# Performance work log

Hardware: AMD Instinct MI355X
Metric: run time of the kernel (lower is better)

## Reference

```python
import jax, jax.numpy as jnp
import numpy as np

B, T, D_IN, D_OUT = 4, 2048, 1024, 1024


def setup_inputs() -> dict:
    key = jax.random.key(0)
    k0, k1, k2, k3 = jax.random.split(key, 4)
    token_embed = jax.random.normal(k0, (B, T, D_IN), dtype=jnp.float32)
    # torch Linear weight is [out, in]; store transposed [in, out] for x @ W
    Wq = jax.random.normal(k1, (D_IN, D_OUT), dtype=jnp.float32) * (1.0 / np.sqrt(D_IN))
    Wk = jax.random.normal(k2, (D_IN, D_OUT), dtype=jnp.float32) * (1.0 / np.sqrt(D_IN))
    Wv = jax.random.normal(k3, (D_IN, D_OUT), dtype=jnp.float32) * (1.0 / np.sqrt(D_IN))
    return {"token_embed": token_embed, "Wq": Wq, "Wk": Wk, "Wv": Wv}


def reference(token_embed, Wq, Wk, Wv):
    # token_embed: [B, T, d_in]
    num_token = token_embed.shape[1]
    q = jnp.einsum("btd,de->bte", token_embed, Wq)  # [B, T, d_out]
    k = jnp.einsum("btd,de->bte", token_embed, Wk)
    v = jnp.einsum("btd,de->bte", token_embed, Wv)
    scores = jnp.einsum("bqe,bke->bqk", q, k)  # [B, T, T]
    # causal mask: strictly-upper-triangular positions set to -inf
    causal = jnp.triu(jnp.ones((num_token, num_token), dtype=bool), k=1)
    scores = jnp.where(causal[None, :, :], -jnp.inf, scores)
    # NOTE: faithful to source bug: scale by sqrt(seq_len) (keys.shape[1]), not sqrt(d_out)
    scale = jnp.asarray(num_token, dtype=scores.dtype) ** 0.5
    attn = jax.nn.softmax(scores / scale, axis=-1)
    # dropout prob is 0 -> identity
    context = jnp.einsum("bqk,bke->bqe", attn, v)  # [B, T, d_out]
    return context
```

## Files before the change

kernel.cpp:

```cpp
#include <hip/hip_runtime.h>
#include <cstdint>
#include <cstddef>
#include <math.h>


typedef __attribute__((ext_vector_type(4))) float f32x4;
typedef __attribute__((ext_vector_type(8))) short s16x8;

#define AS1(p) ((const __attribute__((address_space(1))) void*)(p))
#define AS3(p) ((__attribute__((address_space(3))) void*)(p))
#define BARRIER() asm volatile("s_barrier" ::: "memory")
#define W8 asm volatile("s_waitcnt vmcnt(8)" ::: "memory")
#define W4 asm volatile("s_waitcnt vmcnt(4)" ::: "memory")
#define W0 asm volatile("s_waitcnt vmcnt(0)" ::: "memory")
#define WNONE ((void)0)
#define NOISSUE ((void)0)

static __device__ __forceinline__ unsigned short f2bf(float x) {
  unsigned int u = __float_as_uint(x);
  unsigned int r = u + 0x7FFFu + ((u >> 16) & 1u);
  return (unsigned short)(r >> 16);
}
static __device__ __forceinline__ float bf2f(unsigned short h) {
  return __uint_as_float(((unsigned int)h) << 16);
}

__global__ __launch_bounds__(256) void k_cvtX(const float* __restrict__ X,
                                              unsigned short* __restrict__ Xb) {
  size_t i = ((size_t)blockIdx.x * 256 + threadIdx.x) * 8;
  float4 a = *(const float4*)(X + i);
  float4 b = *(const float4*)(X + i + 4);
  union { unsigned short us[8]; uint4 v; } o;
  o.us[0] = f2bf(a.x); o.us[1] = f2bf(a.y); o.us[2] = f2bf(a.z); o.us[3] = f2bf(a.w);
  o.us[4] = f2bf(b.x); o.us[5] = f2bf(b.y); o.us[6] = f2bf(b.z); o.us[7] = f2bf(b.w);
  *(uint4*)(Xb + i) = o.v;
}

__global__ __launch_bounds__(256) void k_cvtW(const float* __restrict__ W0p,
                                              const float* __restrict__ W1p,
                                              const float* __restrict__ W2p,
                                              unsigned short* __restrict__ Wt) {
  const float* W = blockIdx.z == 0 ? W0p : (blockIdx.z == 1 ? W1p : W2p);
  unsigned short* dst = Wt + (size_t)blockIdx.z * 1024 * 1024;
  __shared__ float tile[64][65];
  int k0 = blockIdx.x * 64, n0 = blockIdx.y * 64;
  int tr = threadIdx.x >> 4, tc = (threadIdx.x & 15) * 4;
  for (int i = 0; i < 4; ++i) {
    int r = tr + i * 16;
    float4 v = *(const float4*)(W + (size_t)(k0 + r) * 1024 + n0 + tc);
    tile[r][tc + 0] = v.x; tile[r][tc + 1] = v.y;
    tile[r][tc + 2] = v.z; tile[r][tc + 3] = v.w;
  }
  __syncthreads();
  for (int i = 0; i < 4; ++i) {
    int r = tr + i * 16;
    ushort4 o;
    o.x = f2bf(tile[tc + 0][r]); o.y = f2bf(tile[tc + 1][r]);
    o.z = f2bf(tile[tc + 2][r]); o.w = f2bf(tile[tc + 3][r]);
    *(ushort4*)(dst + (size_t)(n0 + r) * 1024 + k0 + tc) = o;
  }
}

static __device__ __forceinline__ void stage2(const char* src, size_t ld128, char* dst) {
  __builtin_amdgcn_global_load_lds(AS1(src), AS3(dst), 16, 0, 0);
  __builtin_amdgcn_global_load_lds(AS1(src + ld128), AS3(dst + 8192), 16, 0, 0);
}

template <class FA, class FB>
static __device__ __forceinline__ void core256(const char* __restrict__ As,
                                               const char* __restrict__ Bs,
                                               size_t ldA128, size_t ldB128,
                                               FA offA, FB offB,
                                               int nkt, char* smem, f32x4 (&acc)[8][4]) {
  const int tid = threadIdx.x, w = tid >> 6, lane = tid & 63;
  const int lr = lane & 15, lq = lane >> 4;
  const int wm = (w >> 2) * 128, wn = (w & 3) * 64;
  char* ldsA = smem + w * 1024;
  char* ldsB = smem + 65536 + w * 1024;
  s16x8 af[4], bfr[4];

#define STG_A(t, h) stage2(As + offA((t), (h)), ldA128, ldsA + (((t) & 1) * 2 + (h)) * 16384)
#define STG_B(t, h) stage2(Bs + offB((t), (h)), ldB128, ldsB + (((t) & 1) * 2 + (h)) * 16384)
#define RD_A(buf, h, r) (*(const s16x8*)(smem + ((buf) * 2 + (h)) * 16384 + (r) * 64 + ((lq ^ (((r) >> 1) & 3)) << 4)))
#define RD_B(buf, h, r) (*(const s16x8*)(smem + 65536 + ((buf) * 2 + (h)) * 16384 + (r) * 64 + ((lq ^ (((r) >> 1) & 3)) << 4)))
#define ISS_H1(T) do { STG_A((T) + 1, 1); STG_B((T) + 1, 1); } while (0)
#define ISS_H0(T) do { STG_A((T) + 2, 0); STG_B((T) + 2, 0); } while (0)
#define MFMA_Q(base)                                                                     \
  _Pragma("unroll") for (int i = 0; i < 4; ++i)                                          \
  _Pragma("unroll") for (int c = 0; c < 4; ++c)                                          \
    acc[(base) + i][c] = __builtin_amdgcn_mfma_f32_16x16x32_bf16(af[i], bfr[c], acc[(base) + i][c], 0, 0, 0)
#define PH02(buf, h, ISSUE)                                                              \
  _Pragma("unroll") for (int i = 0; i < 4; ++i) af[i] = RD_A(buf, h, wm + i * 16 + lr);  \
  _Pragma("unroll") for (int c = 0; c < 4; ++c) bfr[c] = RD_B(buf, h, wn + c * 16 + lr); \
  ISSUE; BARRIER();                                                                      \
  __builtin_amdgcn_s_setprio(1); MFMA_Q(0); __builtin_amdgcn_s_setprio(0);               \
  BARRIER();
#define PH13(buf, h, WAIT)                                                               \
  _Pragma("unroll") for (int i = 0; i < 4; ++i) af[i] = RD_A(buf, h, wm + 64 + i * 16 + lr); \
  BARRIER();                                                                             \
  __builtin_amdgcn_s_setprio(1); MFMA_Q(4); __builtin_amdgcn_s_setprio(0);               \
  WAIT; BARRIER();
#define TILE(T, ISS0, ISS2, WAIT1, WAIT3) {                                              \
    const int _buf = (T) & 1;                                                            \
    PH02(_buf, 0, ISS0)                                                                  \
    PH13(_buf, 0, WAIT1)                                                                 \
    PH02(_buf, 1, ISS2)                                                                  \
    PH13(_buf, 1, WAIT3)                                                                 \
  }

  STG_A(0, 0); STG_B(0, 0);
  STG_A(0, 1); STG_B(0, 1);
  STG_A(1, 0); STG_B(1, 0);
  W8; BARRIER();

  int t = 0;
  for (; t + 2 < nkt; ++t) TILE(t, ISS_H1(t), ISS_H0(t), W8, W8)
  TILE(t, ISS_H1(t), NOISSUE, W8, W4)
  ++t;
  TILE(t, NOISSUE, NOISSUE, W0, WNONE)

#undef STG_A
#undef STG_B
#undef RD_A
#undef RD_B
#undef ISS_H1
#undef ISS_H0
#undef MFMA_Q
#undef PH02
#undef PH13
#undef TILE
}

struct OffLinear {
  __device__ __forceinline__ size_t operator()(int t, int h) const {
    return (size_t)t * 128 + (size_t)h * 64;
  }
};
struct OffTri {
  __device__ __forceinline__ size_t operator()(int t, int h) const {
    return (size_t)(t >> 2) * 131072 + (size_t)(t & 3) * 128 + (size_t)h * 64;
  }
};

static __device__ __forceinline__ void lane_src(int ld, int& rowl, int& slot) {
  const int tid = threadIdx.x, w = tid >> 6, lane = tid & 63;
  rowl = w * 16 + (lane >> 2);
  slot = (lane & 3) ^ ((rowl >> 1) & 3);
  (void)ld;
}

__global__ __launch_bounds__(512, 2) void k_qkv(const unsigned short* __restrict__ Xb,
                                                const unsigned short* __restrict__ Wt,
                                                unsigned short* __restrict__ Qm,
                                                unsigned short* __restrict__ Km,
                                                unsigned short* __restrict__ Vt) {
  __shared__ char smem[131072];
  const int by = blockIdx.y, z = by >> 2, q = by & 3, bx = blockIdx.x;
  const char* A; const char* B;
  int m0, n0;
  if (z < 2) {
    m0 = bx * 256; n0 = q * 256;
    A = (const char*)(Xb + (size_t)m0 * 1024);
    B = (const char*)(Wt + (size_t)z * 1048576 + (size_t)n0 * 1024);
  } else {
    m0 = q * 256; n0 = bx * 256;
    A = (const char*)(Wt + (size_t)2 * 1048576 + (size_t)m0 * 1024);
    B = (const char*)(Xb + (size_t)n0 * 1024);
  }
  int rowl, slot; lane_src(2048, rowl, slot);
  const size_t lo = (size_t)rowl * 2048 + slot * 16;
  f32x4 acc[8][4];
#pragma unroll
  for (int i = 0; i < 8; ++i)
#pragma unroll
    for (int c = 0; c < 4; ++c) acc[i][c] = (f32x4){0.f, 0.f, 0.f, 0.f};
  core256(A + lo, B + lo, (size_t)128 * 2048, (size_t)128 * 2048,
          OffLinear{}, OffLinear{}, 16, smem, acc);
  const int tid = threadIdx.x, w = tid >> 6, lane = tid & 63;
  const int lr = lane & 15, lq = lane >> 4;
  const int wm = (w >> 2) * 128, wn = (w & 3) * 64;
#pragma unroll
  for (int fr = 0; fr < 8; ++fr)
#pragma unroll
    for (int fc = 0; fc < 4; ++fc)
#pragma unroll
      for (int i = 0; i < 4; ++i) {
        int row = m0 + wm + fr * 16 + lq * 4 + i;
        int col = n0 + wn + fc * 16 + lr;
        unsigned short hv = f2bf(acc[fr][fc][i]);
        if (z == 0)      Qm[(size_t)row * 1024 + col] = hv;
        else if (z == 1) Km[(size_t)row * 1024 + col] = hv;
        else             Vt[((size_t)(col >> 11) * 1024 + row) * 2048 + (col & 2047)] = hv;
      }
}

__global__ __launch_bounds__(512, 2) void k_sg(const unsigned short* __restrict__ Qm,
                                               const unsigned short* __restrict__ Km,
                                               unsigned short* __restrict__ S) {
  __shared__ char smem[131072];
  const int id = blockIdx.x;
  int i = 0;
  while ((i + 1) * (i + 2) / 2 <= id) ++i;
  const int j = id - i * (i + 1) / 2;
  const int b = blockIdx.y;
  const int m0 = i * 256, n0 = j * 256;
  int rowl, slot; lane_src(2048, rowl, slot);
  const size_t lo = (size_t)rowl * 2048 + slot * 16;
  f32x4 acc[8][4];
#pragma unroll
  for (int a = 0; a < 8; ++a)
#pragma unroll
    for (int c = 0; c < 4; ++c) acc[a][c] = (f32x4){0.f, 0.f, 0.f, 0.f};
  core256((const char*)(Qm + ((size_t)b * 2048 + m0) * 1024) + lo,
          (const char*)(Km + ((size_t)b * 2048 + n0) * 1024) + lo,
          (size_t)128 * 2048, (size_t)128 * 2048, OffLinear{}, OffLinear{}, 16, smem, acc);
  const float SCALE = 0.022097086912079608f;
  const int tid = threadIdx.x, w = tid >> 6, lane = tid & 63;
  const int lr = lane & 15, lq = lane >> 4;
  const int wm = (w >> 2) * 128, wn = (w & 3) * 64;
  unsigned short* tb = S + (((size_t)(b * 36 + id)) << 16);
#pragma unroll
  for (int fr = 0; fr < 8; ++fr)
#pragma unroll
    for (int fc = 0; fc < 4; ++fc)
#pragma unroll
      for (int i2 = 0; i2 < 4; ++i2) {
        int rl = wm + fr * 16 + lq * 4 + i2;
        int cl = wn + fc * 16 + lr;
        tb[(size_t)rl * 256 + cl] = f2bf(acc[fr][fc][i2] * SCALE);
      }
}

__global__ __launch_bounds__(256) void k_softmax(unsigned short* __restrict__ S) {
  const int tid = threadIdx.x, w = tid >> 6, lane = tid & 63;
  const int row = blockIdx.x * 4 + w;
  const int b = row >> 11, q = row & 2047;
  const int i = q >> 8, ntl = i + 1, rowL = q & 255;
  unsigned short* base = S + (((size_t)(b * 36 + (i * (i + 1)) / 2)) << 16)
                           + (size_t)rowL * 256 + lane * 4;
  float v[8][4];
#pragma unroll
  for (int t = 0; t < 8; ++t) {
    if (t < ntl) {
      ushort4 x = *(const ushort4*)(base + (size_t)t * 65536);
      int c0 = t * 256 + lane * 4;
      v[t][0] = (c0 + 0 <= q) ? bf2f(x.x) : -INFINITY;
      v[t][1] = (c0 + 1 <= q) ? bf2f(x.y) : -INFINITY;
      v[t][2] = (c0 + 2 <= q) ? bf2f(x.z) : -INFINITY;
      v[t][3] = (c0 + 3 <= q) ? bf2f(x.w) : -INFINITY;
    } else {
      v[t][0] = v[t][1] = v[t][2] = v[t][3] = -INFINITY;
    }
  }
  float m = -INFINITY;
#pragma unroll
  for (int t = 0; t < 8; ++t)
#pragma unroll
    for (int jj = 0; jj < 4; ++jj) m = fmaxf(m, v[t][jj]);
  for (int off = 32; off; off >>= 1) m = fmaxf(m, __shfl_xor(m, off));
  float s = 0.f;
#pragma unroll
  for (int t = 0; t < 8; ++t)
#pragma unroll
    for (int jj = 0; jj < 4; ++jj) { v[t][jj] = __expf(v[t][jj] - m); s += v[t][jj]; }
  for (int off = 32; off; off >>= 1) s += __shfl_xor(s, off);
  const float inv = 1.f / s;
#pragma unroll
  for (int t = 0; t < 8; ++t)
    if (t < ntl) {
      ushort4 o;
      o.x = f2bf(v[t][0] * inv); o.y = f2bf(v[t][1] * inv);
      o.z = f2bf(v[t][2] * inv); o.w = f2bf(v[t][3] * inv);
      *(ushort4*)(base + (size_t)t * 65536) = o;
    }
}

__global__ __launch_bounds__(512, 2) void k_pv(const unsigned short* __restrict__ P,
                                               const unsigned short* __restrict__ Vt,
                                               float* __restrict__ out) {
  __shared__ char smem[131072];
  const int mtr = 7 - blockIdx.x;
  const int nt = blockIdx.y, b = blockIdx.z;
  const int nkt = (mtr + 1) * 4;
  const char* Pb = (const char*)P + (((size_t)(b * 36 + (mtr * (mtr + 1)) / 2)) << 17);
  int rowl, slot; lane_src(0, rowl, slot);
  const char* Asrc = Pb + (size_t)rowl * 512 + slot * 16;
  const char* Bsrc = (const char*)Vt + ((size_t)(b * 1024 + nt * 256 + rowl)) * 4096 + slot * 16;
  f32x4 acc[8][4];
#pragma unroll
  for (int a = 0; a < 8; ++a)
#pragma unroll
    for (int c = 0; c < 4; ++c) acc[a][c] = (f32x4){0.f, 0.f, 0.f, 0.f};
  core256(Asrc, Bsrc, (size_t)128 * 512, (size_t)128 * 4096,
          OffTri{}, OffLinear{}, nkt, smem, acc);
  const int tid = threadIdx.x, w = tid >> 6, lane = tid & 63;
  const int lr = lane & 15, lq = lane >> 4;
  const int wm = (w >> 2) * 128, wn = (w & 3) * 64;
#pragma unroll
  for (int fr = 0; fr < 8; ++fr)
#pragma unroll
    for (int fc = 0; fc < 4; ++fc)
#pragma unroll
      for (int i2 = 0; i2 < 4; ++i2) {
        int orow = mtr * 256 + wm + fr * 16 + lq * 4 + i2;
        int col = nt * 256 + wn + fc * 16 + lr;
        out[((size_t)b * 2048 + orow) * 1024 + col] = acc[fr][fc][i2];
      }
}

extern "C" void kernel_launch(void* const* d_in, const int* in_sizes, int n_in,
                              void* d_out, int out_size, void* d_ws, size_t ws_size,
                              hipStream_t stream) {
  const float* X  = (const float*)d_in[0];
  const float* W0p = (const float*)d_in[1];
  const float* W1p = (const float*)d_in[2];
  const float* W2p = (const float*)d_in[3];
  float* out = (float*)d_out;
  char* ws = (char*)d_ws;
  unsigned short* Xb = (unsigned short*)ws;
  unsigned short* Wt = (unsigned short*)(ws + (size_t)16777216);
  unsigned short* Qm = (unsigned short*)(ws + (size_t)23068672);
  unsigned short* Km = (unsigned short*)(ws + (size_t)39845888);
  unsigned short* Vt = (unsigned short*)(ws + (size_t)56623104);
  unsigned short* Sb = (unsigned short*)ws;
  (void)in_sizes; (void)n_in; (void)out_size; (void)ws_size;

  hipLaunchKernelGGL(k_cvtX, dim3(4096), dim3(256), 0, stream, X, Xb);
  hipLaunchKernelGGL(k_cvtW, dim3(16, 16, 3), dim3(256), 0, stream, W0p, W1p, W2p, Wt);
  hipLaunchKernelGGL(k_qkv, dim3(32, 12), dim3(512), 0, stream, Xb, Wt, Qm, Km, Vt);
  hipLaunchKernelGGL(k_sg, dim3(36, 4), dim3(512), 0, stream, Qm, Km, Sb);
  hipLaunchKernelGGL(k_softmax, dim3(2048), dim3(256), 0, stream, Sb);
  hipLaunchKernelGGL(k_pv, dim3(8, 4, 4), dim3(512), 0, stream, Sb, Vt, out);
}
```

Baseline: 179.9 us.

## Move V projection into score kernel and split PV over K with atomics

The V projection GEMM moves out of the QKV kernel and into the score-GEMM launch, so the two run concurrently as one grid of 272 blocks (Q/K projection is now 256 blocks). The PV kernel is split along the key dimension into 32 roughly equal chunks per (batch, column tile), using lookup tables, and partial results are accumulated into the output with float atomics after a memset. This balances the triangular causal workload across more CUs and removes the long tail from the largest row tiles. In exchange it adds an output memset, atomic-add traffic, and nondeterministic summation order.

```diff
diff --git a/kernel.cpp b/kernel.cpp
--- a/kernel.cpp
+++ b/kernel.cpp
@@ -136,38 +136,36 @@
     return (size_t)t * 128 + (size_t)h * 64;
   }
 };
-struct OffTri {
+struct OffTriK {
+  int k0;
   __device__ __forceinline__ size_t operator()(int t, int h) const {
-    return (size_t)(t >> 2) * 131072 + (size_t)(t & 3) * 128 + (size_t)h * 64;
+    int g = k0 + t;
+    return (size_t)(g >> 2) * 131072 + (size_t)(g & 3) * 128 + (size_t)h * 64;
   }
 };
-
-static __device__ __forceinline__ void lane_src(int ld, int& rowl, int& slot) {
+struct OffLinK {
+  int k0;
+  __device__ __forceinline__ size_t operator()(int t, int h) const {
+    return (size_t)(k0 + t) * 128 + (size_t)h * 64;
+  }
+};
+
+static __device__ __forceinline__ void lane_src(int& rowl, int& slot) {
   const int tid = threadIdx.x, w = tid >> 6, lane = tid & 63;
   rowl = w * 16 + (lane >> 2);
   slot = (lane & 3) ^ ((rowl >> 1) & 3);
-  (void)ld;
-}
-
-__global__ __launch_bounds__(512, 2) void k_qkv(const unsigned short* __restrict__ Xb,
-                                                const unsigned short* __restrict__ Wt,
-                                                unsigned short* __restrict__ Qm,
-                                                unsigned short* __restrict__ Km,
-                                                unsigned short* __restrict__ Vt) {
+}
+
+__global__ __launch_bounds__(512, 2) void k_qk(const unsigned short* __restrict__ Xb,
+                                               const unsigned short* __restrict__ Wt,
+                                               unsigned short* __restrict__ Qm,
+                                               unsigned short* __restrict__ Km) {
   __shared__ char smem[131072];
   const int by = blockIdx.y, z = by >> 2, q = by & 3, bx = blockIdx.x;
-  const char* A; const char* B;
-  int m0, n0;
-  if (z < 2) {
-    m0 = bx * 256; n0 = q * 256;
-    A = (const char*)(Xb + (size_t)m0 * 1024);
-    B = (const char*)(Wt + (size_t)z * 1048576 + (size_t)n0 * 1024);
-  } else {
-    m0 = q * 256; n0 = bx * 256;
-    A = (const char*)(Wt + (size_t)2 * 1048576 + (size_t)m0 * 1024);
-    B = (const char*)(Xb + (size_t)n0 * 1024);
-  }
-  int rowl, slot; lane_src(2048, rowl, slot);
+  const int m0 = bx * 256, n0 = q * 256;
+  const char* A = (const char*)(Xb + (size_t)m0 * 1024);
+  const char* B = (const char*)(Wt + (size_t)z * 1048576 + (size_t)n0 * 1024);
+  int rowl, slot; lane_src(rowl, slot);
   const size_t lo = (size_t)rowl * 2048 + slot * 16;
   f32x4 acc[8][4];
 #pragma unroll
@@ -176,6 +174,7 @@
     for (int c = 0; c < 4; ++c) acc[i][c] = (f32x4){0.f, 0.f, 0.f, 0.f};
   core256(A + lo, B + lo, (size_t)128 * 2048, (size_t)128 * 2048,
           OffLinear{}, OffLinear{}, 16, smem, acc);
+  unsigned short* C = z == 0 ? Qm : Km;
   const int tid = threadIdx.x, w = tid >> 6, lane = tid & 63;
   const int lr = lane & 15, lq = lane >> 4;
   const int wm = (w >> 2) * 128, wn = (w & 3) * 64;
@@ -187,48 +186,68 @@
       for (int i = 0; i < 4; ++i) {
         int row = m0 + wm + fr * 16 + lq * 4 + i;
         int col = n0 + wn + fc * 16 + lr;
-        unsigned short hv = f2bf(acc[fr][fc][i]);
-        if (z == 0)      Qm[(size_t)row * 1024 + col] = hv;
-        else if (z == 1) Km[(size_t)row * 1024 + col] = hv;
-        else             Vt[((size_t)(col >> 11) * 1024 + row) * 2048 + (col & 2047)] = hv;
+        C[(size_t)row * 1024 + col] = f2bf(acc[fr][fc][i]);
       }
 }
 
-__global__ __launch_bounds__(512, 2) void k_sg(const unsigned short* __restrict__ Qm,
-                                               const unsigned short* __restrict__ Km,
-                                               unsigned short* __restrict__ S) {
+__global__ __launch_bounds__(512, 2) void k_sgv(const unsigned short* __restrict__ Xb,
+                                                const unsigned short* __restrict__ Wt,
+                                                const unsigned short* __restrict__ Qm,
+                                                const unsigned short* __restrict__ Km,
+                                                unsigned short* __restrict__ Vt,
+                                                unsigned short* __restrict__ S) {
   __shared__ char smem[131072];
-  const int id = blockIdx.x;
-  int i = 0;
-  while ((i + 1) * (i + 2) / 2 <= id) ++i;
-  const int j = id - i * (i + 1) / 2;
-  const int b = blockIdx.y;
-  const int m0 = i * 256, n0 = j * 256;
-  int rowl, slot; lane_src(2048, rowl, slot);
+  const int x = blockIdx.x;
+  int rowl, slot; lane_src(rowl, slot);
   const size_t lo = (size_t)rowl * 2048 + slot * 16;
   f32x4 acc[8][4];
 #pragma unroll
   for (int a = 0; a < 8; ++a)
 #pragma unroll
     for (int c = 0; c < 4; ++c) acc[a][c] = (f32x4){0.f, 0.f, 0.f, 0.f};
-  core256((const char*)(Qm + ((size_t)b * 2048 + m0) * 1024) + lo,
-          (const char*)(Km + ((size_t)b * 2048 + n0) * 1024) + lo,
-          (size_t)128 * 2048, (size_t)128 * 2048, OffLinear{}, OffLinear{}, 16, smem, acc);
-  const float SCALE = 0.022097086912079608f;
   const int tid = threadIdx.x, w = tid >> 6, lane = tid & 63;
   const int lr = lane & 15, lq = lane >> 4;
   const int wm = (w >> 2) * 128, wn = (w & 3) * 64;
-  unsigned short* tb = S + (((size_t)(b * 36 + id)) << 16);
-#pragma unroll
-  for (int fr = 0; fr < 8; ++fr)
-#pragma unroll
-    for (int fc = 0; fc < 4; ++fc)
-#pragma unroll
-      for (int i2 = 0; i2 < 4; ++i2) {
-        int rl = wm + fr * 16 + lq * 4 + i2;
-        int cl = wn + fc * 16 + lr;
-        tb[(size_t)rl * 256 + cl] = f2bf(acc[fr][fc][i2] * SCALE);
-      }
+
+  if (x < 128) {
+    const int m0 = (x & 3) * 256, n0 = (x >> 2) * 256;
+    const char* A = (const char*)(Wt + (size_t)2 * 1048576 + (size_t)m0 * 1024);
+    const char* B = (const char*)(Xb + (size_t)n0 * 1024);
+    core256(A + lo, B + lo, (size_t)128 * 2048, (size_t)128 * 2048,
+            OffLinear{}, OffLinear{}, 16, smem, acc);
+#pragma unroll
+    for (int fr = 0; fr < 8; ++fr)
+#pragma unroll
+      for (int fc = 0; fc < 4; ++fc)
+#pragma unroll
+        for (int i = 0; i < 4; ++i) {
+          int row = m0 + wm + fr * 16 + lq * 4 + i;
+          int col = n0 + wn + fc * 16 + lr;
+          Vt[((size_t)(col >> 11) * 1024 + row) * 2048 + (col & 2047)] = f2bf(acc[fr][fc][i]);
+        }
+  } else {
+    const int id2 = x - 128;
+    const int b = id2 / 36, id = id2 % 36;
+    int i = 0;
+    while ((i + 1) * (i + 2) / 2 <= id) ++i;
+    const int j = id - i * (i + 1) / 2;
+    const int m0 = i * 256, n0 = j * 256;
+    core256((const char*)(Qm + ((size_t)b * 2048 + m0) * 1024) + lo,
+            (const char*)(Km + ((size_t)b * 2048 + n0) * 1024) + lo,
+            (size_t)128 * 2048, (size_t)128 * 2048, OffLinear{}, OffLinear{}, 16, smem, acc);
+    const float SCALE = 0.022097086912079608f;
+    unsigned short* tb = S + (((size_t)(b * 36 + id)) << 16);
+#pragma unroll
+    for (int fr = 0; fr < 8; ++fr)
+#pragma unroll
+      for (int fc = 0; fc < 4; ++fc)
+#pragma unroll
+        for (int i2 = 0; i2 < 4; ++i2) {
+          int rl = wm + fr * 16 + lq * 4 + i2;
+          int cl = wn + fc * 16 + lr;
+          tb[(size_t)rl * 256 + cl] = f2bf(acc[fr][fc][i2] * SCALE);
+        }
+  }
 }
 
 __global__ __launch_bounds__(256) void k_softmax(unsigned short* __restrict__ S) {
@@ -275,15 +294,19 @@
     }
 }
 
+__device__ const int pv_i[32]  = {7,7,7,7,7,7,7, 6,6,6,6,6,6, 5,5,5,5,5, 4,4,4,4, 3,3,3,3, 2,2,2, 1,1, 0};
+__device__ const int pv_k0[32] = {0,5,10,15,20,24,28, 0,5,10,15,20,24, 0,5,10,15,20, 0,5,10,15, 0,4,8,12, 0,4,8, 0,4, 0};
+__device__ const int pv_nk[32] = {5,5,5,5,4,4,4, 5,5,5,5,4,4, 5,5,5,5,4, 5,5,5,5, 4,4,4,4, 4,4,4, 4,4, 4};
+
 __global__ __launch_bounds__(512, 2) void k_pv(const unsigned short* __restrict__ P,
                                                const unsigned short* __restrict__ Vt,
                                                float* __restrict__ out) {
   __shared__ char smem[131072];
-  const int mtr = 7 - blockIdx.x;
-  const int nt = blockIdx.y, b = blockIdx.z;
-  const int nkt = (mtr + 1) * 4;
-  const char* Pb = (const char*)P + (((size_t)(b * 36 + (mtr * (mtr + 1)) / 2)) << 17);
-  int rowl, slot; lane_src(0, rowl, slot);
+  const int cx = blockIdx.x & 31;
+  const int nt = (blockIdx.x >> 5) & 3, b = blockIdx.x >> 7;
+  const int i = pv_i[cx], k0 = pv_k0[cx], nkt = pv_nk[cx];
+  const char* Pb = (const char*)P + (((size_t)(b * 36 + (i * (i + 1)) / 2)) << 17);
+  int rowl, slot; lane_src(rowl, slot);
   const char* Asrc = Pb + (size_t)rowl * 512 + slot * 16;
   const char* Bsrc = (const char*)Vt + ((size_t)(b * 1024 + nt * 256 + rowl)) * 4096 + slot * 16;
   f32x4 acc[8][4];
@@ -292,7 +315,7 @@
 #pragma unroll
     for (int c = 0; c < 4; ++c) acc[a][c] = (f32x4){0.f, 0.f, 0.f, 0.f};
   core256(Asrc, Bsrc, (size_t)128 * 512, (size_t)128 * 4096,
-          OffTri{}, OffLinear{}, nkt, smem, acc);
+          OffTriK{k0}, OffLinK{k0}, nkt, smem, acc);
   const int tid = threadIdx.x, w = tid >> 6, lane = tid & 63;
   const int lr = lane & 15, lq = lane >> 4;
   const int wm = (w >> 2) * 128, wn = (w & 3) * 64;
@@ -302,9 +325,9 @@
     for (int fc = 0; fc < 4; ++fc)
 #pragma unroll
       for (int i2 = 0; i2 < 4; ++i2) {
-        int orow = mtr * 256 + wm + fr * 16 + lq * 4 + i2;
+        int orow = i * 256 + wm + fr * 16 + lq * 4 + i2;
         int col = nt * 256 + wn + fc * 16 + lr;
-        out[((size_t)b * 2048 + orow) * 1024 + col] = acc[fr][fc][i2];
+        unsafeAtomicAdd(out + ((size_t)b * 2048 + orow) * 1024 + col, acc[fr][fc][i2]);
       }
 }
 
@@ -323,12 +346,13 @@
   unsigned short* Km = (unsigned short*)(ws + (size_t)39845888);
   unsigned short* Vt = (unsigned short*)(ws + (size_t)56623104);
   unsigned short* Sb = (unsigned short*)ws;
-  (void)in_sizes; (void)n_in; (void)out_size; (void)ws_size;
-
+  (void)in_sizes; (void)n_in; (void)ws_size;
+
+  hipMemsetAsync(out, 0, (size_t)out_size * sizeof(float), stream);
   hipLaunchKernelGGL(k_cvtX, dim3(4096), dim3(256), 0, stream, X, Xb);
   hipLaunchKernelGGL(k_cvtW, dim3(16, 16, 3), dim3(256), 0, stream, W0p, W1p, W2p, Wt);
-  hipLaunchKernelGGL(k_qkv, dim3(32, 12), dim3(512), 0, stream, Xb, Wt, Qm, Km, Vt);
-  hipLaunchKernelGGL(k_sg, dim3(36, 4), dim3(512), 0, stream, Qm, Km, Sb);
+  hipLaunchKernelGGL(k_qk, dim3(32, 8), dim3(512), 0, stream, Xb, Wt, Qm, Km);
+  hipLaunchKernelGGL(k_sgv, dim3(272), dim3(512), 0, stream, Xb, Wt, Qm, Km, Vt, Sb);
   hipLaunchKernelGGL(k_softmax, dim3(2048), dim3(256), 0, stream, Sb);
-  hipLaunchKernelGGL(k_pv, dim3(8, 4, 4), dim3(512), 0, stream, Sb, Vt, out);
-}
+  hipLaunchKernelGGL(k_pv, dim3(512), dim3(512), 0, stream, Sb, Vt, out);
+}
```

New measurement: 246.0 us. 1.37x slower.
